# Performance work log

Measured on AMD Instinct MI355X. Metric: run time of the kernel, lower is better.

## Reference

```python
import jax, jax.numpy as jnp
import numpy as np
import math

B, S, D, H, F, L, V = 2, 2048, 1024, 16, 4096, 3, 32000
DK = D // H
EPS = 1e-6
NEG = -1e9


def layernorm(x, a, b):
    # torch: std(-1) is Bessel-corrected (ddof=1); eps added to std, not var
    mean = x.mean(-1, keepdims=True)
    std = jnp.sqrt(((x - mean) ** 2).sum(-1, keepdims=True) / (x.shape[-1] - 1))
    return a * (x - mean) / (std + EPS) + b


def setup_inputs() -> dict:
    key = jax.random.key(0)
    ks = jax.random.split(key, 12)
    rn = lambda k, shape, s=0.02: jax.random.normal(k, shape, dtype=jnp.float32) * s
    tokens = jax.random.randint(ks[0], (B, S), 0, V, dtype=jnp.int32)
    mask = jnp.ones((B, 1, S), dtype=jnp.int32)
    emb = rn(ks[1], (V, D), 1.0)
    # sinusoidal positional encoding (buffer, matches PositionalEncoding)
    pos = np.arange(S, dtype=np.float32)[:, None]
    div = np.exp(np.arange(0, D, 2, dtype=np.float32) * -(math.log(10000.0) / D))
    pe_np = np.zeros((S, D), np.float32)
    pe_np[:, 0::2] = np.sin(pos * div)
    pe_np[:, 1::2] = np.cos(pos * div)
    pe = jnp.asarray(pe_np)
    return dict(
        tokens=tokens, mask=mask, emb=emb, pe=pe,
        Wq=rn(ks[2], (L, D, D)), bq=jnp.zeros((L, D), jnp.float32),
        Wk=rn(ks[3], (L, D, D)), bk=jnp.zeros((L, D), jnp.float32),
        Wv=rn(ks[4], (L, D, D)), bv=jnp.zeros((L, D), jnp.float32),
        Wo=rn(ks[5], (L, D, D)), bo=jnp.zeros((L, D), jnp.float32),
        w1=rn(ks[6], (L, D, F)), b1=jnp.zeros((L, F), jnp.float32),
        w2=rn(ks[7], (L, F, D)), b2=jnp.zeros((L, D), jnp.float32),
        ln_a=jnp.ones((L, 2, D), jnp.float32), ln_b=jnp.zeros((L, 2, D), jnp.float32),
        fa=jnp.ones((D,), jnp.float32), fb=jnp.zeros((D,), jnp.float32),
    )


def encoder(tokens, mask, emb, pe, Wq, bq, Wk, bk, Wv, bv, Wo, bo,
            w1, b1, w2, b2, ln_a, ln_b, fa, fb):
    x = emb[tokens] * jnp.float32(math.sqrt(D)) + pe[None, :, :]  # [B,S,D]
    m = (mask[:, None, :, :] != 0)  # [B,1,1,S] broadcast over heads and queries
    scale = jnp.float32(1.0 / math.sqrt(DK))
    for l in range(L):
        # --- self-attention sublayer (pre-LN residual) ---
        h = layernorm(x, ln_a[l, 0], ln_b[l, 0])
        q = (h @ Wq[l] + bq[l]).reshape(B, S, H, DK)
        k = (h @ Wk[l] + bk[l]).reshape(B, S, H, DK)
        v = (h @ Wv[l] + bv[l]).reshape(B, S, H, DK)
        scores = jnp.einsum('bqhd,bkhd->bhqk', q, k) * scale
        scores = jnp.where(m, scores, jnp.float32(NEG))
        p = jax.nn.softmax(scores, axis=-1)
        o = jnp.einsum('bhqk,bkhd->bqhd', p, v).reshape(B, S, D)
        x = x + (o @ Wo[l] + bo[l])
        # --- feed-forward sublayer (pre-LN residual) ---
        h = layernorm(x, ln_a[l, 1], ln_b[l, 1])
        x = x + (jax.nn.relu(h @ w1[l] + b1[l]) @ w2[l] + b2[l])
    return layernorm(x, fa, fb)


def reference(tokens, mask, emb, pe, Wq, bq, Wk, bk, Wv, bv, Wo, bo,
              w1, b1, w2, b2, ln_a, ln_b, fa, fb):
    return encoder(tokens, mask, emb, pe, Wq, bq, Wk, bk, Wv, bv, Wo, bo,
                   w1, b1, w2, b2, ln_a, ln_b, fa, fb)
```

## Files before the change

kernel.cpp:

```cpp
#include <hip/hip_runtime.h>
#include <math.h>
#include <stdint.h>

constexpr int kB = 2, kS = 2048, kD = 1024, kH = 16, kF = 4096, kL = 3;
constexpr int kDK = 64;
constexpr int kQKV = 3 * kD;

typedef __attribute__((ext_vector_type(8))) short short8;
typedef __attribute__((ext_vector_type(4))) float floatx4;

__device__ inline float bf2f(unsigned short u) {
  union { uint32_t i; float f; } v; v.i = (uint32_t)u << 16; return v.f;
}
__device__ inline unsigned short f2bf(float x) {
  union { float f; uint32_t i; } v; v.f = x;
  uint32_t r = v.i + 0x7fffu + ((v.i >> 16) & 1u);
  return (unsigned short)(r >> 16);
}

__device__ inline void dma16(const void* g, void* l) {
  __builtin_amdgcn_global_load_lds(
      (const __attribute__((address_space(1))) unsigned int*)g,
      (__attribute__((address_space(3))) unsigned int*)l, 16, 0, 0);
}

__global__ __launch_bounds__(256) void embed_kernel(
    const int* __restrict__ tokens, const float* __restrict__ emb,
    const float* __restrict__ pe, float* __restrict__ x)
{
  int i = blockIdx.x;
  int s = i & (kS - 1);
  int tok = tokens[i];
  const float4* ep = (const float4*)(emb + (size_t)tok * kD);
  const float4* pp = (const float4*)(pe + (size_t)s * kD);
  float4* xp = (float4*)(x + (size_t)i * kD);
  int t = threadIdx.x;
  float4 e = ep[t], p = pp[t];
  xp[t] = make_float4(e.x*32.0f + p.x, e.y*32.0f + p.y,
                      e.z*32.0f + p.z, e.w*32.0f + p.w);
}

__global__ __launch_bounds__(256) void ln_kernel(
    const float* __restrict__ x, const float* __restrict__ ga,
    const float* __restrict__ gb, float* __restrict__ out)
{
  int row = blockIdx.x;
  int t = threadIdx.x;
  int lane = t & 63, wid = t >> 6;
  const float4* xp = (const float4*)(x + (size_t)row * kD);
  float4 v = xp[t];
  float s = v.x + v.y + v.z + v.w;
  #pragma unroll
  for (int o = 32; o; o >>= 1) s += __shfl_xor(s, o);
  __shared__ float red[4];
  if (lane == 0) red[wid] = s;
  __syncthreads();
  float mean = (red[0] + red[1] + red[2] + red[3]) * (1.0f / 1024.0f);
  float4 d = make_float4(v.x - mean, v.y - mean, v.z - mean, v.w - mean);
  float ss = d.x*d.x + d.y*d.y + d.z*d.z + d.w*d.w;
  #pragma unroll
  for (int o = 32; o; o >>= 1) ss += __shfl_xor(ss, o);
  __syncthreads();
  if (lane == 0) red[wid] = ss;
  __syncthreads();
  float var = (red[0] + red[1] + red[2] + red[3]) * (1.0f / 1023.0f);
  float inv = 1.0f / (sqrtf(var) + 1e-6f);
  float4 a4 = ((const float4*)ga)[t];
  float4 b4 = ((const float4*)gb)[t];
  float4 o4;
  o4.x = a4.x * d.x * inv + b4.x;
  o4.y = a4.y * d.y * inv + b4.y;
  o4.z = a4.z * d.z * inv + b4.z;
  o4.w = a4.w * d.w * inv + b4.w;
  ((float4*)(out + (size_t)row * kD))[t] = o4;
}

__global__ __launch_bounds__(256) void ln_split_kernel(
    const float* __restrict__ x, const float* __restrict__ ga,
    const float* __restrict__ gb, unsigned short* __restrict__ hi,
    unsigned short* __restrict__ lo)
{
  int row = blockIdx.x;
  int t = threadIdx.x;
  int lane = t & 63, wid = t >> 6;
  const float4* xp = (const float4*)(x + (size_t)row * kD);
  float4 v = xp[t];
  float s = v.x + v.y + v.z + v.w;
  #pragma unroll
  for (int o = 32; o; o >>= 1) s += __shfl_xor(s, o);
  __shared__ float red[4];
  if (lane == 0) red[wid] = s;
  __syncthreads();
  float mean = (red[0] + red[1] + red[2] + red[3]) * (1.0f / 1024.0f);
  float4 d = make_float4(v.x - mean, v.y - mean, v.z - mean, v.w - mean);
  float ss = d.x*d.x + d.y*d.y + d.z*d.z + d.w*d.w;
  #pragma unroll
  for (int o = 32; o; o >>= 1) ss += __shfl_xor(ss, o);
  __syncthreads();
  if (lane == 0) red[wid] = ss;
  __syncthreads();
  float var = (red[0] + red[1] + red[2] + red[3]) * (1.0f / 1023.0f);
  float inv = 1.0f / (sqrtf(var) + 1e-6f);
  float4 a4 = ((const float4*)ga)[t];
  float4 b4 = ((const float4*)gb)[t];
  float o0 = a4.x * d.x * inv + b4.x;
  float o1 = a4.y * d.y * inv + b4.y;
  float o2 = a4.z * d.z * inv + b4.z;
  float o3 = a4.w * d.w * inv + b4.w;
  ushort4 h4, l4;
  h4.x = f2bf(o0); l4.x = f2bf(o0 - bf2f(h4.x));
  h4.y = f2bf(o1); l4.y = f2bf(o1 - bf2f(h4.y));
  h4.z = f2bf(o2); l4.z = f2bf(o2 - bf2f(h4.z));
  h4.w = f2bf(o3); l4.w = f2bf(o3 - bf2f(h4.w));
  *(ushort4*)&hi[(size_t)row * kD + 4*t] = h4;
  *(ushort4*)&lo[(size_t)row * kD + 4*t] = l4;
}

__global__ __launch_bounds__(256) void wconv_kernel(
    const float* __restrict__ W, unsigned short* __restrict__ hi,
    unsigned short* __restrict__ lo, int K, int N)
{
  __shared__ float tile[64][65];
  int n0 = blockIdx.x * 64, k0 = blockIdx.y * 64;
  int c = threadIdx.x & 63, r0 = threadIdx.x >> 6;
  #pragma unroll
  for (int p = 0; p < 16; ++p) {
    int r = r0 + 4 * p;
    tile[r][c] = W[(size_t)(k0 + r) * N + n0 + c];
  }
  __syncthreads();
  #pragma unroll
  for (int p = 0; p < 16; ++p) {
    int nn = r0 + 4 * p;
    float xv = tile[c][nn];
    unsigned short h = f2bf(xv);
    size_t o = (size_t)(n0 + nn) * K + k0 + c;
    hi[o] = h;
    lo[o] = f2bf(xv - bf2f(h));
  }
}

template<int TERMS, int OUTMODE>
__global__ __launch_bounds__(256, 3) void mfma_gemm(
    const unsigned short* __restrict__ Ahi, const unsigned short* __restrict__ Alo,
    const unsigned short* __restrict__ Whi, const unsigned short* __restrict__ Wlo,
    const float* __restrict__ bias, const float* __restrict__ resid,
    void* __restrict__ out, int M, int N, int K)
{
  __shared__ unsigned short sAhi[128 * 32];
  __shared__ unsigned short sBhi[128 * 32];
  __shared__ unsigned short sBlo[128 * 32];
  __shared__ unsigned short sAlo[TERMS == 3 ? 128 * 32 : 64];

  int t = threadIdx.x;
  int lane = t & 63, wv = t >> 6;
  int wm = (wv >> 1) * 64, wn = (wv & 1) * 64;
  int lr = lane & 15, lq = lane >> 4;
  int m0 = blockIdx.y * 128, n0 = blockIdx.x * 128;

  int u = lane >> 2;
  int kq_g = (lane & 3) ^ ((u ^ (u >> 2)) & 3);
  int swv = (lr ^ (lr >> 2)) & 3;

  floatx4 acc[4][4];
  #pragma unroll
  for (int i = 0; i < 4; ++i)
    #pragma unroll
    for (int j = 0; j < 4; ++j) acc[i][j] = (floatx4){0.f, 0.f, 0.f, 0.f};

  for (int k0 = 0; k0 < K; k0 += 32) {
    __syncthreads();
    #pragma unroll
    for (int p = 0; p < 2; ++p) {
      int W = 2 * wv + p;
      size_t ga = (size_t)(m0 + 16 * W + u) * K + k0 + 8 * kq_g;
      size_t gb = (size_t)(n0 + 16 * W + u) * K + k0 + 8 * kq_g;
      dma16(&Ahi[ga], &sAhi[W * 512]);
      if (TERMS == 3) dma16(&Alo[ga], &sAlo[W * 512]);
      dma16(&Whi[gb], &sBhi[W * 512]);
      dma16(&Wlo[gb], &sBlo[W * 512]);
    }
    __syncthreads();

    short8 ah[4], bh[4];
    #pragma unroll
    for (int i = 0; i < 4; ++i)
      ah[i] = *(const short8*)&sAhi[(wm + 16*i + lr) * 32 + 8 * (lq ^ swv)];
    #pragma unroll
    for (int j = 0; j < 4; ++j)
      bh[j] = *(const short8*)&sBhi[(wn + 16*j + lr) * 32 + 8 * (lq ^ swv)];
    #pragma unroll
    for (int i = 0; i < 4; ++i)
      #pragma unroll
      for (int j = 0; j < 4; ++j)
        acc[i][j] = __builtin_amdgcn_mfma_f32_16x16x32_bf16(ah[i], bh[j], acc[i][j], 0, 0, 0);

    short8 bl[4];
    #pragma unroll
    for (int j = 0; j < 4; ++j)
      bl[j] = *(const short8*)&sBlo[(wn + 16*j + lr) * 32 + 8 * (lq ^ swv)];
    #pragma unroll
    for (int i = 0; i < 4; ++i)
      #pragma unroll
      for (int j = 0; j < 4; ++j)
        acc[i][j] = __builtin_amdgcn_mfma_f32_16x16x32_bf16(ah[i], bl[j], acc[i][j], 0, 0, 0);

    if (TERMS == 3) {
      short8 al[4];
      #pragma unroll
      for (int i = 0; i < 4; ++i)
        al[i] = *(const short8*)&sAlo[(wm + 16*i + lr) * 32 + 8 * (lq ^ swv)];
      #pragma unroll
      for (int i = 0; i < 4; ++i)
        #pragma unroll
        for (int j = 0; j < 4; ++j)
          acc[i][j] = __builtin_amdgcn_mfma_f32_16x16x32_bf16(al[i], bh[j], acc[i][j], 0, 0, 0);
    }
  }

  #pragma unroll
  for (int i = 0; i < 4; ++i) {
    #pragma unroll
    for (int j = 0; j < 4; ++j) {
      int col = n0 + wn + 16*j + lr;
      float bv = bias[col];
      #pragma unroll
      for (int r = 0; r < 4; ++r) {
        int row = m0 + wm + 16*i + 4*lq + r;
        float val = acc[i][j][r] + bv;
        if (OUTMODE == 0) {
          if (resid) val += resid[(size_t)row * N + col];
          ((float*)out)[(size_t)row * N + col] = val;
        } else if (OUTMODE == 1) {
          ((unsigned short*)out)[(size_t)row * N + col] = f2bf(fmaxf(val, 0.f));
        } else {
          ((unsigned short*)out)[(size_t)row * N + col] = f2bf(val);
        }
      }
    }
  }
}

#define ASTR 72

__global__ __launch_bounds__(256) void attn_kernel(
    const unsigned short* __restrict__ Qg, const unsigned short* __restrict__ Kg,
    const unsigned short* __restrict__ Vg, const int* __restrict__ mask,
    unsigned short* __restrict__ oHi, unsigned short* __restrict__ oLo, int ldq)
{
  __shared__ unsigned short Qs[128 * ASTR];
  __shared__ unsigned short Ks[64 * ASTR];
  __shared__ unsigned short Vs[64 * ASTR];
  __shared__ unsigned short Ps[128 * ASTR];

  int bi = blockIdx.x;
  int qt = bi & 15;
  int h  = (bi >> 4) & 15;
  int b  = bi >> 8;
  int q0 = qt * 128;
  int t = threadIdx.x;
  int lane = t & 63, wv = t >> 6;
  int lr = lane & 15, lq = lane >> 4;
  int wq = wv * 32;

  const size_t hin  = (size_t)b * kS * ldq + (size_t)h * kDK;
  const size_t hout = (size_t)b * kS * kD  + (size_t)h * kDK;

  #pragma unroll
  for (int p = 0; p < 4; ++p) {
    int c = t + 256 * p;
    int row = c >> 3, dq = c & 7;
    *(uint4*)&Qs[row * ASTR + 8 * dq] =
        *(const uint4*)&Qg[hin + (size_t)(q0 + row) * ldq + 8 * dq];
  }

  floatx4 Oacc[2][4];
  float m_i[2][4], l_i[2][4];
  #pragma unroll
  for (int i = 0; i < 2; ++i)
    #pragma unroll
    for (int r = 0; r < 4; ++r) {
      m_i[i][r] = -3.0e38f; l_i[i][r] = 0.0f;
    }
  #pragma unroll
  for (int i = 0; i < 2; ++i)
    #pragma unroll
    for (int j = 0; j < 4; ++j) Oacc[i][j] = (floatx4){0.f, 0.f, 0.f, 0.f};

  for (int k0 = 0; k0 < kS; k0 += 64) {
    __syncthreads();

    #pragma unroll
    for (int p = 0; p < 2; ++p) {
      int c = t + 256 * p;
      int row = c >> 3, dq = c & 7;
      size_t g = hin + (size_t)(k0 + row) * ldq + 8 * dq;
      *(uint4*)&Ks[row * ASTR + 8 * dq] = *(const uint4*)&Kg[g];
      uint4 vv = *(const uint4*)&Vg[g];
      const unsigned short* vs = (const unsigned short*)&vv;
      #pragma unroll
      for (int j = 0; j < 8; ++j)
        Vs[(8 * dq + j) * ASTR + row] = vs[j];
    }
    int mv[4];
    #pragma unroll
    for (int j = 0; j < 4; ++j) mv[j] = mask[b * kS + k0 + 16*j + lr];
    __syncthreads();

    floatx4 sac[2][4];
    #pragma unroll
    for (int i = 0; i < 2; ++i)
      #pragma unroll
      for (int j = 0; j < 4; ++j) sac[i][j] = (floatx4){0.f, 0.f, 0.f, 0.f};
    #pragma unroll
    for (int ks = 0; ks < 2; ++ks) {
      short8 af[2], bf[4];
      #pragma unroll
      for (int i = 0; i < 2; ++i)
        af[i] = *(const short8*)&Qs[(wq + 16*i + lr) * ASTR + 32*ks + 8*lq];
      #pragma unroll
      for (int j = 0; j < 4; ++j)
        bf[j] = *(const short8*)&Ks[(16*j + lr) * ASTR + 32*ks + 8*lq];
      #pragma unroll
      for (int i = 0; i < 2; ++i)
        #pragma unroll
        for (int j = 0; j < 4; ++j)
          sac[i][j] = __builtin_amdgcn_mfma_f32_16x16x32_bf16(af[i], bf[j], sac[i][j], 0, 0, 0);
    }

    #pragma unroll
    for (int i = 0; i < 2; ++i)
      #pragma unroll
      for (int j = 0; j < 4; ++j) {
        #pragma unroll
        for (int r = 0; r < 4; ++r) sac[i][j][r] *= 0.125f;
        if (mv[j] == 0)
          #pragma unroll
          for (int r = 0; r < 4; ++r) sac[i][j][r] = -1e9f;
      }

    float alf[2][4];
    #pragma unroll
    for (int i = 0; i < 2; ++i)
      #pragma unroll
      for (int r = 0; r < 4; ++r) {
        float mx = fmaxf(fmaxf(sac[i][0][r], sac[i][1][r]),
                         fmaxf(sac[i][2][r], sac[i][3][r]));
        #pragma unroll
        for (int o = 1; o < 16; o <<= 1) mx = fmaxf(mx, __shfl_xor(mx, o));
        float newm = fmaxf(m_i[i][r], mx);
        float rs = 0.0f;
        #pragma unroll
        for (int j = 0; j < 4; ++j) {
          float e = __expf(sac[i][j][r] - newm);
          sac[i][j][r] = e; rs += e;
        }
        #pragma unroll
        for (int o = 1; o < 16; o <<= 1) rs += __shfl_xor(rs, o);
        alf[i][r] = __expf(m_i[i][r] - newm);
        l_i[i][r] = l_i[i][r] * alf[i][r] + rs;
        m_i[i][r] = newm;
      }

    #pragma unroll
    for (int i = 0; i < 2; ++i)
      #pragma unroll
      for (int j = 0; j < 4; ++j)
        #pragma unroll
        for (int r = 0; r < 4; ++r)
          Ps[(wq + 16*i + 4*lq + r) * ASTR + 16*j + lr] = f2bf(sac[i][j][r]);

    #pragma unroll
    for (int i = 0; i < 2; ++i)
      #pragma unroll
      for (int j = 0; j < 4; ++j)
        #pragma unroll
        for (int r = 0; r < 4; ++r) Oacc[i][j][r] *= alf[i][r];

    #pragma unroll
    for (int ks = 0; ks < 2; ++ks) {
      short8 pa[2], vb[4];
      #pragma unroll
      for (int i = 0; i < 2; ++i)
        pa[i] = *(const short8*)&Ps[(wq + 16*i + lr) * ASTR + 32*ks + 8*lq];
      #pragma unroll
      for (int j = 0; j < 4; ++j)
        vb[j] = *(const short8*)&Vs[(16*j + lr) * ASTR + 32*ks + 8*lq];
      #pragma unroll
      for (int i = 0; i < 2; ++i)
        #pragma unroll
        for (int j = 0; j < 4; ++j)
          Oacc[i][j] = __builtin_amdgcn_mfma_f32_16x16x32_bf16(pa[i], vb[j], Oacc[i][j], 0, 0, 0);
    }
  }

  #pragma unroll
  for (int i = 0; i < 2; ++i) {
    float inv[4];
    #pragma unroll
    for (int r = 0; r < 4; ++r) inv[r] = 1.0f / l_i[i][r];
    #pragma unroll
    for (int j = 0; j < 4; ++j)
      #pragma unroll
      for (int r = 0; r < 4; ++r) {
        int row = q0 + wq + 16*i + 4*lq + r;
        float val = Oacc[i][j][r] * inv[r];
        unsigned short hv = f2bf(val);
        unsigned short lv = f2bf(val - bf2f(hv));
        size_t addr = hout + (size_t)row * kD + 16*j + lr;
        oHi[addr] = hv;
        oLo[addr] = lv;
      }
  }
}

extern "C" void kernel_launch(void* const* d_in, const int* in_sizes, int n_in,
                              void* d_out, int out_size, void* d_ws, size_t ws_size,
                              hipStream_t stream) {
  const int*   tokens = (const int*)d_in[0];
  const int*   mask   = (const int*)d_in[1];
  const float* emb    = (const float*)d_in[2];
  const float* pe     = (const float*)d_in[3];
  const float* Wq     = (const float*)d_in[4];
  const float* bq     = (const float*)d_in[5];
  const float* Wk     = (const float*)d_in[6];
  const float* bk     = (const float*)d_in[7];
  const float* Wv     = (const float*)d_in[8];
  const float* bv     = (const float*)d_in[9];
  const float* Wo     = (const float*)d_in[10];
  const float* bo     = (const float*)d_in[11];
  const float* w1     = (const float*)d_in[12];
  const float* b1     = (const float*)d_in[13];
  const float* w2     = (const float*)d_in[14];
  const float* b2     = (const float*)d_in[15];
  const float* ln_a   = (const float*)d_in[16];
  const float* ln_b   = (const float*)d_in[17];
  const float* fa     = (const float*)d_in[18];
  const float* fb     = (const float*)d_in[19];
  float* out = (float*)d_out;
  char*  ws  = (char*)d_ws;

  const int T = kB * kS;
  constexpr size_t MB = 1024 * 1024;

  float*          x     = (float*)(ws);
  unsigned short* hHi   = (unsigned short*)(ws + 16 * MB);
  unsigned short* hLo   = (unsigned short*)(ws + 24 * MB);
  unsigned short* qkv   = (unsigned short*)(ws + 32 * MB);
  float*          bqkv  = (float*)(ws + 56 * MB);
  unsigned short* fpln  = (unsigned short*)(ws + 32 * MB);
  char*           Wbuf  = ws + 64 * MB;

  unsigned short* qkv_hi = (unsigned short*)(Wbuf);
  unsigned short* qkv_lo = (unsigned short*)(Wbuf + 6 * MB);
  unsigned short* so_hi  = (unsigned short*)(Wbuf + 12 * MB);
  unsigned short* so_lo  = (unsigned short*)(Wbuf + 14 * MB);
  unsigned short* ffn_hi = (unsigned short*)(Wbuf + 16 * MB);
  unsigned short* ffn_lo = (unsigned short*)(Wbuf + 24 * MB);

  dim3 blk(256);
  embed_kernel<<<T, blk, 0, stream>>>(tokens, emb, pe, x);

  for (int l = 0; l < kL; ++l) {
    const float* Wql = Wq + (size_t)l * kD * kD;
    const float* Wkl = Wk + (size_t)l * kD * kD;
    const float* Wvl = Wv + (size_t)l * kD * kD;
    const float* Wol = Wo + (size_t)l * kD * kD;
    const float* w1l = w1 + (size_t)l * kD * kF;
    const float* w2l = w2 + (size_t)l * kF * kD;

    wconv_kernel<<<dim3(kD/64, kD/64), blk, 0, stream>>>(
        Wql, qkv_hi,                 qkv_lo,                 kD, kD);
    wconv_kernel<<<dim3(kD/64, kD/64), blk, 0, stream>>>(
        Wkl, qkv_hi + (size_t)kD*kD, qkv_lo + (size_t)kD*kD, kD, kD);
    wconv_kernel<<<dim3(kD/64, kD/64), blk, 0, stream>>>(
        Wvl, qkv_hi + (size_t)2*kD*kD, qkv_lo + (size_t)2*kD*kD, kD, kD);
    wconv_kernel<<<dim3(kD/64, kD/64), blk, 0, stream>>>(Wol, so_hi, so_lo, kD, kD);
    hipMemcpyAsync(bqkv,          bq + (size_t)l*kD, kD*4, hipMemcpyDeviceToDevice, stream);
    hipMemcpyAsync(bqkv + kD,     bk + (size_t)l*kD, kD*4, hipMemcpyDeviceToDevice, stream);
    hipMemcpyAsync(bqkv + 2*kD,   bv + (size_t)l*kD, kD*4, hipMemcpyDeviceToDevice, stream);

    ln_split_kernel<<<T, blk, 0, stream>>>(x, ln_a + (size_t)l * 2 * kD,
                                           ln_b + (size_t)l * 2 * kD, hHi, hLo);
    mfma_gemm<3,2><<<dim3(kQKV/128, T/128), blk, 0, stream>>>(
        hHi, hLo, qkv_hi, qkv_lo, bqkv, nullptr, qkv, T, kQKV, kD);
    attn_kernel<<<kB * kH * (kS / 128), blk, 0, stream>>>(
        qkv, qkv + kD, qkv + 2*kD, mask, hHi, hLo, kQKV);
    mfma_gemm<3,0><<<dim3(kD/128, T/128), blk, 0, stream>>>(
        hHi, hLo, so_hi, so_lo, bo + (size_t)l * kD, x, x, T, kD, kD);

    ln_split_kernel<<<T, blk, 0, stream>>>(x, ln_a + (size_t)l * 2 * kD + kD,
                                           ln_b + (size_t)l * 2 * kD + kD, hHi, hLo);
    wconv_kernel<<<dim3(kF/64, kD/64), blk, 0, stream>>>(w1l, ffn_hi, ffn_lo, kD, kF);
    mfma_gemm<3,1><<<dim3(kF/128, T/128), blk, 0, stream>>>(
        hHi, hLo, ffn_hi, ffn_lo, b1 + (size_t)l * kF, nullptr, fpln, T, kF, kD);
    wconv_kernel<<<dim3(kD/64, kF/64), blk, 0, stream>>>(w2l, ffn_hi, ffn_lo, kF, kD);
    mfma_gemm<2,0><<<dim3(kD/128, T/128), blk, 0, stream>>>(
        fpln, nullptr, ffn_hi, ffn_lo, b2 + (size_t)l * kD, x, x, T, kD, kF);
  }

  ln_kernel<<<T, blk, 0, stream>>>(x, fa, fb, out);
}
```

Measured before the change: 2.013 ms.

## Write V transposed from QKV GEMM and retile attention with DMA swizzled loads

The QKV GEMM gets a new epilogue mode that writes Q and K into a packed 2048-wide buffer and writes V pre-transposed per head, so the attention kernel no longer transposes V with scalar LDS stores. The attention kernel switches to 64-query tiles with one 16-row strip per wave, loads Q, K and V with global_load_lds DMA into XOR-swizzled LDS tiles, and requests higher occupancy through launch bounds. The aim is to cut LDS transpose and bank-conflict overhead and to raise occupancy. In exchange, each 64-query block reloads the full K and V stream, doubling that global traffic, and the GEMM epilogue now does scattered 8-byte stores for V.

New measurement: 1.867 ms. 7.2% less time.

```diff
diff --git a/kernel.cpp b/kernel.cpp
--- a/kernel.cpp
+++ b/kernel.cpp
@@ -218,6 +218,35 @@
     }
   }
 
+  if (OUTMODE == 3) {
+    unsigned short* qk  = (unsigned short*)out;
+    unsigned short* vTp = (unsigned short*)resid;
+    #pragma unroll
+    for (int i = 0; i < 4; ++i) {
+      #pragma unroll
+      for (int j = 0; j < 4; ++j) {
+        int col = n0 + wn + 16*j + lr;
+        float bv = bias[col];
+        int row0 = m0 + wm + 16*i + 4*lq;
+        if (col < 2048) {
+          #pragma unroll
+          for (int r = 0; r < 4; ++r)
+            qk[(size_t)(row0 + r) * 2048 + col] = f2bf(acc[i][j][r] + bv);
+        } else {
+          ushort4 w;
+          w.x = f2bf(acc[i][j][0] + bv);
+          w.y = f2bf(acc[i][j][1] + bv);
+          w.z = f2bf(acc[i][j][2] + bv);
+          w.w = f2bf(acc[i][j][3] + bv);
+          int bb = row0 >> 11, s0 = row0 & 2047;
+          int hh = (col - 2048) >> 6, dk = (col - 2048) & 63;
+          *(ushort4*)&vTp[((size_t)((bb << 4) + hh) * 64 + dk) * 2048 + s0] = w;
+        }
+      }
+    }
+    return;
+  }
+
   #pragma unroll
   for (int i = 0; i < 4; ++i) {
     #pragma unroll
@@ -243,175 +272,148 @@
 
 #define ASTR 72
 
-__global__ __launch_bounds__(256) void attn_kernel(
-    const unsigned short* __restrict__ Qg, const unsigned short* __restrict__ Kg,
-    const unsigned short* __restrict__ Vg, const int* __restrict__ mask,
-    unsigned short* __restrict__ oHi, unsigned short* __restrict__ oLo, int ldq)
+__global__ __launch_bounds__(256, 4) void attn_kernel(
+    const unsigned short* __restrict__ QKg, const unsigned short* __restrict__ vT,
+    const int* __restrict__ mask, unsigned short* __restrict__ oHi,
+    unsigned short* __restrict__ oLo)
 {
-  __shared__ unsigned short Qs[128 * ASTR];
-  __shared__ unsigned short Ks[64 * ASTR];
-  __shared__ unsigned short Vs[64 * ASTR];
-  __shared__ unsigned short Ps[128 * ASTR];
+  __shared__ unsigned short Qs[64 * 64];
+  __shared__ unsigned short Ks[64 * 64];
+  __shared__ unsigned short Vs[64 * 64];
+  __shared__ unsigned short Ps[64 * ASTR];
 
   int bi = blockIdx.x;
-  int qt = bi & 15;
-  int h  = (bi >> 4) & 15;
-  int b  = bi >> 8;
-  int q0 = qt * 128;
+  int bh = bi & 31;
+  int qt = bi >> 5;
+  int h = bh & 15, b = bh >> 4;
+  int q0 = qt * 64;
   int t = threadIdx.x;
   int lane = t & 63, wv = t >> 6;
   int lr = lane & 15, lq = lane >> 4;
-  int wq = wv * 32;
-
-  const size_t hin  = (size_t)b * kS * ldq + (size_t)h * kDK;
-  const size_t hout = (size_t)b * kS * kD  + (size_t)h * kDK;
-
-  #pragma unroll
-  for (int p = 0; p < 4; ++p) {
-    int c = t + 256 * p;
-    int row = c >> 3, dq = c & 7;
-    *(uint4*)&Qs[row * ASTR + 8 * dq] =
-        *(const uint4*)&Qg[hin + (size_t)(q0 + row) * ldq + 8 * dq];
-  }
-
-  floatx4 Oacc[2][4];
-  float m_i[2][4], l_i[2][4];
-  #pragma unroll
-  for (int i = 0; i < 2; ++i)
-    #pragma unroll
-    for (int r = 0; r < 4; ++r) {
-      m_i[i][r] = -3.0e38f; l_i[i][r] = 0.0f;
-    }
-  #pragma unroll
-  for (int i = 0; i < 2; ++i)
-    #pragma unroll
-    for (int j = 0; j < 4; ++j) Oacc[i][j] = (floatx4){0.f, 0.f, 0.f, 0.f};
+  int wq = wv * 16;
+
+  const size_t qbase = (size_t)b * kS * 2048 + (size_t)h * kDK;
+  const size_t kbase = qbase + 1024;
+  const size_t vbase = (size_t)(b * kH + h) * 64 * 2048;
+  const size_t hout  = (size_t)b * kS * kD + (size_t)h * kDK;
+
+  #pragma unroll
+  for (int p = 0; p < 2; ++p) {
+    int idx = t + 256 * p;
+    int row = idx >> 3, cg = (idx & 7) ^ (row & 7);
+    dma16(&QKg[qbase + (size_t)(q0 + row) * 2048 + 8 * cg],
+          &Qs[(p * 256 + wv * 64) * 8]);
+  }
+
+  floatx4 Oacc[4];
+  float m_i[4], l_i[4];
+  #pragma unroll
+  for (int r = 0; r < 4; ++r) { m_i[r] = -3.0e38f; l_i[r] = 0.0f; }
+  #pragma unroll
+  for (int j = 0; j < 4; ++j) Oacc[j] = (floatx4){0.f, 0.f, 0.f, 0.f};
 
   for (int k0 = 0; k0 < kS; k0 += 64) {
     __syncthreads();
-
     #pragma unroll
     for (int p = 0; p < 2; ++p) {
-      int c = t + 256 * p;
-      int row = c >> 3, dq = c & 7;
-      size_t g = hin + (size_t)(k0 + row) * ldq + 8 * dq;
-      *(uint4*)&Ks[row * ASTR + 8 * dq] = *(const uint4*)&Kg[g];
-      uint4 vv = *(const uint4*)&Vg[g];
-      const unsigned short* vs = (const unsigned short*)&vv;
-      #pragma unroll
-      for (int j = 0; j < 8; ++j)
-        Vs[(8 * dq + j) * ASTR + row] = vs[j];
+      int idx = t + 256 * p;
+      int row = idx >> 3, cg = (idx & 7) ^ (row & 7);
+      dma16(&QKg[kbase + (size_t)(k0 + row) * 2048 + 8 * cg],
+            &Ks[(p * 256 + wv * 64) * 8]);
+      dma16(&vT[vbase + (size_t)row * 2048 + k0 + 8 * cg],
+            &Vs[(p * 256 + wv * 64) * 8]);
     }
     int mv[4];
     #pragma unroll
     for (int j = 0; j < 4; ++j) mv[j] = mask[b * kS + k0 + 16*j + lr];
     __syncthreads();
 
-    floatx4 sac[2][4];
-    #pragma unroll
-    for (int i = 0; i < 2; ++i)
-      #pragma unroll
-      for (int j = 0; j < 4; ++j) sac[i][j] = (floatx4){0.f, 0.f, 0.f, 0.f};
+    floatx4 sac[4];
+    #pragma unroll
+    for (int j = 0; j < 4; ++j) sac[j] = (floatx4){0.f, 0.f, 0.f, 0.f};
     #pragma unroll
     for (int ks = 0; ks < 2; ++ks) {
-      short8 af[2], bf[4];
-      #pragma unroll
-      for (int i = 0; i < 2; ++i)
-        af[i] = *(const short8*)&Qs[(wq + 16*i + lr) * ASTR + 32*ks + 8*lq];
+      int cs = ((4 * ks + lq) ^ (lr & 7)) * 8;
+      short8 af = *(const short8*)&Qs[(wq + lr) * 64 + cs];
+      short8 bf[4];
       #pragma unroll
       for (int j = 0; j < 4; ++j)
-        bf[j] = *(const short8*)&Ks[(16*j + lr) * ASTR + 32*ks + 8*lq];
-      #pragma unroll
-      for (int i = 0; i < 2; ++i)
+        bf[j] = *(const short8*)&Ks[(16*j + lr) * 64 + cs];
+      #pragma unroll
+      for (int j = 0; j < 4; ++j)
+        sac[j] = __builtin_amdgcn_mfma_f32_16x16x32_bf16(af, bf[j], sac[j], 0, 0, 0);
+    }
+
+    #pragma unroll
+    for (int j = 0; j < 4; ++j) {
+      #pragma unroll
+      for (int r = 0; r < 4; ++r) sac[j][r] *= 0.125f;
+      if (mv[j] == 0)
         #pragma unroll
-        for (int j = 0; j < 4; ++j)
-          sac[i][j] = __builtin_amdgcn_mfma_f32_16x16x32_bf16(af[i], bf[j], sac[i][j], 0, 0, 0);
-    }
-
-    #pragma unroll
-    for (int i = 0; i < 2; ++i)
+        for (int r = 0; r < 4; ++r) sac[j][r] = -1e9f;
+    }
+
+    float alf[4];
+    #pragma unroll
+    for (int r = 0; r < 4; ++r) {
+      float mx = fmaxf(fmaxf(sac[0][r], sac[1][r]),
+                       fmaxf(sac[2][r], sac[3][r]));
+      #pragma unroll
+      for (int o = 1; o < 16; o <<= 1) mx = fmaxf(mx, __shfl_xor(mx, o));
+      float newm = fmaxf(m_i[r], mx);
+      float rs = 0.0f;
       #pragma unroll
       for (int j = 0; j < 4; ++j) {
-        #pragma unroll
-        for (int r = 0; r < 4; ++r) sac[i][j][r] *= 0.125f;
-        if (mv[j] == 0)
-          #pragma unroll
-          for (int r = 0; r < 4; ++r) sac[i][j][r] = -1e9f;
+        float e = __expf(sac[j][r] - newm);
+        sac[j][r] = e; rs += e;
       }
-
-    float alf[2][4];
-    #pragma unroll
-    for (int i = 0; i < 2; ++i)
-      #pragma unroll
-      for (int r = 0; r < 4; ++r) {
-        float mx = fmaxf(fmaxf(sac[i][0][r], sac[i][1][r]),
-                         fmaxf(sac[i][2][r], sac[i][3][r]));
-        #pragma unroll
-        for (int o = 1; o < 16; o <<= 1) mx = fmaxf(mx, __shfl_xor(mx, o));
-        float newm = fmaxf(m_i[i][r], mx);
-        float rs = 0.0f;
-        #pragma unroll
-        for (int j = 0; j < 4; ++j) {
-          float e = __expf(sac[i][j][r] - newm);
-          sac[i][j][r] = e; rs += e;
-        }
-        #pragma unroll
-        for (int o = 1; o < 16; o <<= 1) rs += __shfl_xor(rs, o);
-        alf[i][r] = __expf(m_i[i][r] - newm);
-        l_i[i][r] = l_i[i][r] * alf[i][r] + rs;
-        m_i[i][r] = newm;
-      }
-
-    #pragma unroll
-    for (int i = 0; i < 2; ++i)
+      #pragma unroll
+      for (int o = 1; o < 16; o <<= 1) rs += __shfl_xor(rs, o);
+      alf[r] = __expf(m_i[r] - newm);
+      l_i[r] = l_i[r] * alf[r] + rs;
+      m_i[r] = newm;
+    }
+
+    #pragma unroll
+    for (int j = 0; j < 4; ++j)
+      #pragma unroll
+      for (int r = 0; r < 4; ++r)
+        Ps[(wq + 4*lq + r) * ASTR + 16*j + lr] = f2bf(sac[j][r]);
+
+    #pragma unroll
+    for (int j = 0; j < 4; ++j)
+      #pragma unroll
+      for (int r = 0; r < 4; ++r) Oacc[j][r] *= alf[r];
+
+    #pragma unroll
+    for (int ks = 0; ks < 2; ++ks) {
+      int cs = ((4 * ks + lq) ^ (lr & 7)) * 8;
+      short8 pa = *(const short8*)&Ps[(wq + lr) * ASTR + 32*ks + 8*lq];
+      short8 vb[4];
       #pragma unroll
       for (int j = 0; j < 4; ++j)
-        #pragma unroll
-        for (int r = 0; r < 4; ++r)
-          Ps[(wq + 16*i + 4*lq + r) * ASTR + 16*j + lr] = f2bf(sac[i][j][r]);
-
-    #pragma unroll
-    for (int i = 0; i < 2; ++i)
+        vb[j] = *(const short8*)&Vs[(16*j + lr) * 64 + cs];
       #pragma unroll
       for (int j = 0; j < 4; ++j)
-        #pragma unroll
-        for (int r = 0; r < 4; ++r) Oacc[i][j][r] *= alf[i][r];
-
-    #pragma unroll
-    for (int ks = 0; ks < 2; ++ks) {
-      short8 pa[2], vb[4];
-      #pragma unroll
-      for (int i = 0; i < 2; ++i)
-        pa[i] = *(const short8*)&Ps[(wq + 16*i + lr) * ASTR + 32*ks + 8*lq];
-      #pragma unroll
-      for (int j = 0; j < 4; ++j)
-        vb[j] = *(const short8*)&Vs[(16*j + lr) * ASTR + 32*ks + 8*lq];
-      #pragma unroll
-      for (int i = 0; i < 2; ++i)
-        #pragma unroll
-        for (int j = 0; j < 4; ++j)
-          Oacc[i][j] = __builtin_amdgcn_mfma_f32_16x16x32_bf16(pa[i], vb[j], Oacc[i][j], 0, 0, 0);
-    }
-  }
-
-  #pragma unroll
-  for (int i = 0; i < 2; ++i) {
-    float inv[4];
-    #pragma unroll
-    for (int r = 0; r < 4; ++r) inv[r] = 1.0f / l_i[i][r];
-    #pragma unroll
-    for (int j = 0; j < 4; ++j)
-      #pragma unroll
-      for (int r = 0; r < 4; ++r) {
-        int row = q0 + wq + 16*i + 4*lq + r;
-        float val = Oacc[i][j][r] * inv[r];
-        unsigned short hv = f2bf(val);
-        unsigned short lv = f2bf(val - bf2f(hv));
-        size_t addr = hout + (size_t)row * kD + 16*j + lr;
-        oHi[addr] = hv;
-        oLo[addr] = lv;
-      }
-  }
+        Oacc[j] = __builtin_amdgcn_mfma_f32_16x16x32_bf16(pa, vb[j], Oacc[j], 0, 0, 0);
+    }
+  }
+
+  float inv[4];
+  #pragma unroll
+  for (int r = 0; r < 4; ++r) inv[r] = 1.0f / l_i[r];
+  #pragma unroll
+  for (int j = 0; j < 4; ++j)
+    #pragma unroll
+    for (int r = 0; r < 4; ++r) {
+      int row = q0 + wq + 4*lq + r;
+      float val = Oacc[j][r] * inv[r];
+      unsigned short hv = f2bf(val);
+      unsigned short lv = f2bf(val - bf2f(hv));
+      size_t addr = hout + (size_t)row * kD + 16*j + lr;
+      oHi[addr] = hv;
+      oLo[addr] = lv;
+    }
 }
 
 extern "C" void kernel_launch(void* const* d_in, const int* in_sizes, int n_in,
@@ -446,7 +448,8 @@
   float*          x     = (float*)(ws);
   unsigned short* hHi   = (unsigned short*)(ws + 16 * MB);
   unsigned short* hLo   = (unsigned short*)(ws + 24 * MB);
-  unsigned short* qkv   = (unsigned short*)(ws + 32 * MB);
+  unsigned short* qk    = (unsigned short*)(ws + 32 * MB);
+  unsigned short* vT    = (unsigned short*)(ws + 48 * MB);
   float*          bqkv  = (float*)(ws + 56 * MB);
   unsigned short* fpln  = (unsigned short*)(ws + 32 * MB);
   char*           Wbuf  = ws + 64 * MB;
@@ -482,10 +485,10 @@
 
     ln_split_kernel<<<T, blk, 0, stream>>>(x, ln_a + (size_t)l * 2 * kD,
                                            ln_b + (size_t)l * 2 * kD, hHi, hLo);
-    mfma_gemm<3,2><<<dim3(kQKV/128, T/128), blk, 0, stream>>>(
-        hHi, hLo, qkv_hi, qkv_lo, bqkv, nullptr, qkv, T, kQKV, kD);
-    attn_kernel<<<kB * kH * (kS / 128), blk, 0, stream>>>(
-        qkv, qkv + kD, qkv + 2*kD, mask, hHi, hLo, kQKV);
+    mfma_gemm<3,3><<<dim3(kQKV/128, T/128), blk, 0, stream>>>(
+        hHi, hLo, qkv_hi, qkv_lo, bqkv, (const float*)vT, qk, T, kQKV, kD);
+    attn_kernel<<<kB * kH * (kS / 64), blk, 0, stream>>>(
+        qk, vT, mask, hHi, hLo);
     mfma_gemm<3,0><<<dim3(kD/128, T/128), blk, 0, stream>>>(
         hHi, hLo, so_hi, so_lo, bo + (size_t)l * kD, x, x, T, kD, kD);
 
```
